# Optimization experiments

Measured on AMD Instinct MI355X. Metric: run time of the kernel, lower is better.

Reference implementation:

```python
import jax, jax.numpy as jnp
import numpy as np
from jax import lax

EPS = 1e-5
K = 32
S1, S2 = 512, 256


def bn_relu(x, gamma, beta, axes):
    # BatchNorm in training mode (batch statistics, biased variance) + ReLU.
    mean = jnp.mean(x, axis=axes, keepdims=True)
    var = jnp.var(x, axis=axes, keepdims=True)
    return jax.nn.relu((x - mean) * lax.rsqrt(var + EPS) * gamma + beta)


def fps(xyz, s):
    # Farthest point sampling, deterministic start at index 0. xyz: [N,3] -> [s] indices
    N = xyz.shape[0]
    def body(carry, _):
        dist, far = carry
        d = jnp.sum((xyz - xyz[far]) ** 2, axis=-1)
        dist = jnp.minimum(dist, d)
        return (dist, jnp.argmax(dist).astype(jnp.int32)), far
    init = (jnp.full((N,), 1e10, xyz.dtype), jnp.int32(0))
    _, idx = lax.scan(body, init, None, length=s)
    return idx


def sample_and_knn_group(s, k, coords, features):
    # coords: [B,N,3], features: [B,N,D]
    fps_idx = jax.vmap(lambda c: fps(c, s))(coords)                      # [B,s]
    new_xyz = jnp.take_along_axis(coords, fps_idx[..., None], axis=1)   # [B,s,3]
    new_feat = jnp.take_along_axis(features, fps_idx[..., None], axis=1)  # [B,s,D]
    # squared euclidean distances [B,s,N]
    d2 = (jnp.sum(new_xyz ** 2, -1)[..., None]
          - 2.0 * jnp.einsum('bsc,bnc->bsn', new_xyz, coords)
          + jnp.sum(coords ** 2, -1)[:, None, :])
    _, knn_idx = lax.top_k(-d2, k)                                       # [B,s,k]
    grouped = jax.vmap(lambda f, i: f[i])(features, knn_idx)             # [B,s,k,D]
    rel = grouped - new_feat[:, :, None, :]
    agg = jnp.concatenate([rel, jnp.broadcast_to(new_feat[:, :, None, :], rel.shape)], axis=-1)  # [B,s,k,2D]
    return new_xyz, agg


def sg_block(s, coords, feats, w1, cb1, g1, b1, w2, cb2, g2, b2):
    new_xyz, agg = sample_and_knn_group(s, K, coords, feats)
    h = bn_relu(jnp.einsum('bskc,oc->bsko', agg, w1) + cb1, g1, b1, (0, 1, 2))
    h = bn_relu(jnp.einsum('bskc,oc->bsko', h, w2) + cb2, g2, b2, (0, 1, 2))
    return new_xyz, jnp.max(h, axis=2)  # max over k neighbors -> [B,s,O]


def setup_inputs() -> dict:
    key = jax.random.key(0)
    ks = jax.random.split(key, 8)
    B, N = 16, 2048
    sc = 0.05
    return {
        'x': jax.random.normal(ks[0], (B, 3, N), jnp.float32),
        'emb_w1': jax.random.normal(ks[1], (64, 3), jnp.float32) * sc,
        'emb_g1': jnp.ones((64,), jnp.float32), 'emb_b1': jnp.zeros((64,), jnp.float32),
        'emb_w2': jax.random.normal(ks[2], (64, 64), jnp.float32) * sc,
        'emb_g2': jnp.ones((64,), jnp.float32), 'emb_b2': jnp.zeros((64,), jnp.float32),
        'sg1_w1': jax.random.normal(ks[3], (128, 128), jnp.float32) * sc,
        'sg1_cb1': jnp.zeros((128,), jnp.float32),
        'sg1_g1': jnp.ones((128,), jnp.float32), 'sg1_b1': jnp.zeros((128,), jnp.float32),
        'sg1_w2': jax.random.normal(ks[4], (128, 128), jnp.float32) * sc,
        'sg1_cb2': jnp.zeros((128,), jnp.float32),
        'sg1_g2': jnp.ones((128,), jnp.float32), 'sg1_b2': jnp.zeros((128,), jnp.float32),
        'sg2_w1': jax.random.normal(ks[5], (512, 256), jnp.float32) * sc,
        'sg2_cb1': jnp.zeros((512,), jnp.float32),
        'sg2_g1': jnp.ones((512,), jnp.float32), 'sg2_b1': jnp.zeros((512,), jnp.float32),
        'sg2_w2': jax.random.normal(ks[6], (512, 512), jnp.float32) * sc,
        'sg2_cb2': jnp.zeros((512,), jnp.float32),
        'sg2_g2': jnp.ones((512,), jnp.float32), 'sg2_b2': jnp.zeros((512,), jnp.float32),
    }


def reference(x, emb_w1, emb_g1, emb_b1, emb_w2, emb_g2, emb_b2,
              sg1_w1, sg1_cb1, sg1_g1, sg1_b1, sg1_w2, sg1_cb2, sg1_g2, sg1_b2,
              sg2_w1, sg2_cb1, sg2_g1, sg2_b1, sg2_w2, sg2_cb2, sg2_g2, sg2_b2):
    xyz = jnp.transpose(x, (0, 2, 1))  # [B,N,3]
    f = bn_relu(jnp.einsum('bnc,oc->bno', xyz, emb_w1), emb_g1, emb_b1, (0, 1))   # [B,N,64]
    f = bn_relu(jnp.einsum('bnc,oc->bno', f, emb_w2), emb_g2, emb_b2, (0, 1))
    xyz1, f1 = sg_block(S1, xyz, f, sg1_w1, sg1_cb1, sg1_g1, sg1_b1,
                        sg1_w2, sg1_cb2, sg1_g2, sg1_b2)   # [B,512,128]
    _, f2 = sg_block(S2, xyz1, f1, sg2_w1, sg2_cb1, sg2_g1, sg2_b1,
                     sg2_w2, sg2_cb2, sg2_g2, sg2_b2)      # [B,256,512]
    return jnp.transpose(f2, (0, 2, 1))  # [B,512,256] to match torch [B,C,s]
```

## Files before the change

### kernel.cpp

```cpp
#include <hip/hip_runtime.h>
#include <hip/hip_bf16.h>

#define EPS_BN 1e-5f
constexpr int BB = 16, NN = 2048, SS1 = 512, SS2 = 256, KNb = 32;

typedef short bf16x8 __attribute__((ext_vector_type(8)));
typedef float f32x4 __attribute__((ext_vector_type(4)));

__device__ inline float bflo(unsigned u) { return __uint_as_float(u << 16); }
__device__ inline float bfhi(unsigned u) { return __uint_as_float(u & 0xffff0000u); }
__device__ inline unsigned short f2bf_bits(float v) {
  __hip_bfloat16 h = __float2bfloat16(v);
  return *reinterpret_cast<unsigned short*>(&h);
}
__device__ inline unsigned fmono(float v) {
  int b = __float_as_int(v);
  return (unsigned)(b ^ ((b >> 31) | 0x80000000));
}

template <int CTRL>
__device__ inline void dpp_step_min(unsigned& hi, unsigned& lo) {
  unsigned hs = (unsigned)__builtin_amdgcn_update_dpp((int)hi, (int)hi, CTRL, 0xF, 0xF, false);
  unsigned ls = (unsigned)__builtin_amdgcn_update_dpp((int)lo, (int)lo, CTRL, 0xF, 0xF, false);
  bool take = (hs < hi) || (hs == hi && ls < lo);
  hi = take ? hs : hi; lo = take ? ls : lo;
}
template <int CTRL>
__device__ inline void dpp_step_maxv_minidx(unsigned& hi, unsigned& lo) {
  unsigned hs = (unsigned)__builtin_amdgcn_update_dpp((int)hi, (int)hi, CTRL, 0xF, 0xF, false);
  unsigned ls = (unsigned)__builtin_amdgcn_update_dpp((int)lo, (int)lo, CTRL, 0xF, 0xF, false);
  bool take = (hs > hi) || (hs == hi && ls < lo);
  hi = take ? hs : hi; lo = take ? ls : lo;
}
__device__ inline void dpp_chain_min(unsigned& hi, unsigned& lo) {
  dpp_step_min<0x111>(hi, lo); dpp_step_min<0x112>(hi, lo);
  dpp_step_min<0x114>(hi, lo); dpp_step_min<0x118>(hi, lo);
  dpp_step_min<0x142>(hi, lo); dpp_step_min<0x143>(hi, lo);
}
__device__ inline void dpp_chain_maxv_minidx(unsigned& hi, unsigned& lo) {
  dpp_step_maxv_minidx<0x111>(hi, lo); dpp_step_maxv_minidx<0x112>(hi, lo);
  dpp_step_maxv_minidx<0x114>(hi, lo); dpp_step_maxv_minidx<0x118>(hi, lo);
  dpp_step_maxv_minidx<0x142>(hi, lo); dpp_step_maxv_minidx<0x143>(hi, lo);
}
__device__ inline int dpp_reduce_min_idx(unsigned hi, unsigned lo) {
  dpp_chain_min(hi, lo);
  return __builtin_amdgcn_readlane((int)lo, 63);
}

__global__ void k_transpose(const float* __restrict__ x, float* __restrict__ xyz) {
  int idx = blockIdx.x * blockDim.x + threadIdx.x;
  if (idx >= BB * NN * 3) return;
  int c = idx % 3; int n = (idx / 3) % NN; int b = idx / (3 * NN);
  xyz[idx] = x[((size_t)b * 3 + c) * NN + n];
}

__global__ void k_emb1(const float* __restrict__ xyz, const float* __restrict__ w,
                       float* __restrict__ out) {
  int idx = blockIdx.x * blockDim.x + threadIdx.x;
  if (idx >= BB * NN * 64) return;
  int o = idx & 63; int pt = idx >> 6;
  const float* p = xyz + (size_t)pt * 3;
  const float* wr = w + o * 3;
  out[idx] = p[0] * wr[0] + p[1] * wr[1] + p[2] * wr[2];
}

__global__ void k_emb2(const float* __restrict__ fin, const float* __restrict__ w,
                       float* __restrict__ out) {
  int idx = blockIdx.x * blockDim.x + threadIdx.x;
  if (idx >= BB * NN * 64) return;
  int o = idx & 63; int pt = idx >> 6;
  const float* f = fin + (size_t)pt * 64;
  const float* wr = w + o * 64;
  float acc = 0.f;
#pragma unroll
  for (int c = 0; c < 64; c++) acc += f[c] * wr[c];
  out[idx] = acc;
}

template <int O>
__global__ void k_stats_direct(const float* __restrict__ data, int rows,
                               const float* __restrict__ gamma, const float* __restrict__ beta,
                               float* __restrict__ scale, float* __restrict__ shift) {
  int o = blockIdx.x; int t = threadIdx.x;
  double s = 0.0, s2 = 0.0;
  for (int r = t; r < rows; r += 256) {
    float v = data[(size_t)r * O + o];
    s += v; s2 += (double)v * (double)v;
  }
  __shared__ double ls[256], ls2[256];
  ls[t] = s; ls2[t] = s2; __syncthreads();
  for (int off = 128; off > 0; off >>= 1) {
    if (t < off) { ls[t] += ls[t + off]; ls2[t] += ls2[t + off]; }
    __syncthreads();
  }
  if (t == 0) {
    double mean = ls[0] / rows;
    double var = ls2[0] / rows - mean * mean;
    float sc = gamma[o] * rsqrtf((float)var + EPS_BN);
    scale[o] = sc; shift[o] = beta[o] - (float)mean * sc;
  }
}

__global__ void k_normrelu(float* __restrict__ data, const float* __restrict__ scale,
                           const float* __restrict__ shift, int total, int O) {
  int idx = blockIdx.x * blockDim.x + threadIdx.x;
  if (idx >= total) return;
  int o = idx % O;
  data[idx] = fmaxf(data[idx] * scale[o] + shift[o], 0.f);
}

template <int N>
__global__ __launch_bounds__(256, 1) void k_fps_mw(const float* __restrict__ xyz, int S,
                                                   int* __restrict__ fpsidx,
                                                   float* __restrict__ newxyz) {
  constexpr int PPL = N / 256;
  int b = blockIdx.x; int t = threadIdx.x;
  int w = t >> 6;
  __shared__ float sx[N], sy[N], sz[N];
  __shared__ unsigned combH[2][4], combL[2][4];
  float px[PPL], py[PPL], pz[PPL], ds[PPL];
#pragma unroll
  for (int r = 0; r < PPL; r++) {
    int i = r * 256 + t;
    size_t base = ((size_t)b * N + i) * 3;
    float xx = xyz[base], yy = xyz[base + 1], zz = xyz[base + 2];
    px[r] = xx; py[r] = yy; pz[r] = zz;
    float ox = xx, oy = yy, oz = zz;
    asm volatile("" : "+v"(ox), "+v"(oy), "+v"(oz));
    sx[i] = ox; sy[i] = oy; sz[i] = oz;
    ds[r] = 1e10f;
  }
  __syncthreads();
  int far = 0; int p = 0;
  for (int it = 0; it < S; it++) {
    float fx = sx[far], fy = sy[far], fz = sz[far];
    if (t == 0) {
      fpsidx[b * S + it] = far;
      size_t ob = ((size_t)b * S + it) * 3;
      newxyz[ob] = fx; newxyz[ob + 1] = fy; newxyz[ob + 2] = fz;
    }
    float mm0 = -1.f, mm1 = -1.f, mm2 = -1.f, mm3 = -1.f;
#pragma unroll
    for (int r = 0; r < PPL; r++) {
      float dx = px[r] - fx, dy = py[r] - fy, dz = pz[r] - fz;
      float d = dx * dx + dy * dy + dz * dz;
      float nd = d < ds[r] ? d : ds[r];
      ds[r] = nd;
      if ((r & 3) == 0) mm0 = nd > mm0 ? nd : mm0;
      else if ((r & 3) == 1) mm1 = nd > mm1 ? nd : mm1;
      else if ((r & 3) == 2) mm2 = nd > mm2 ? nd : mm2;
      else mm3 = nd > mm3 ? nd : mm3;
    }
    float m = fmaxf(fmaxf(mm0, mm1), fmaxf(mm2, mm3));
    int cand[PPL];
#pragma unroll
    for (int r = 0; r < PPL; r++) cand[r] = (ds[r] == m) ? (r * 256 + t) : 0x7fffffff;
#pragma unroll
    for (int st = PPL / 2; st > 0; st >>= 1)
#pragma unroll
      for (int r = 0; r < st; r++) cand[r] = cand[r] < cand[r + st] ? cand[r] : cand[r + st];
    unsigned hi = fmono(m), lo = (unsigned)cand[0];
    dpp_chain_maxv_minidx(hi, lo);
    unsigned rh = (unsigned)__builtin_amdgcn_readlane((int)hi, 63);
    unsigned rl = (unsigned)__builtin_amdgcn_readlane((int)lo, 63);
    combH[p][w] = rh;
    combL[p][w] = rl;
    __syncthreads();
    unsigned bh = combH[p][0], bl = combL[p][0];
#pragma unroll
    for (int ww = 1; ww < 4; ww++) {
      unsigned oh = combH[p][ww], ol = combL[p][ww];
      bool take = (oh > bh) || (oh == bh && ol < bl);
      bh = take ? oh : bh; bl = take ? ol : bl;
    }
    far = (int)bl;
    p ^= 1;
  }
}

template <int N, int S>
__global__ __launch_bounds__(64, 1) void k_knn_wave(const float* __restrict__ pts,
                                                    const float* __restrict__ ctr,
                                                    int* __restrict__ knn) {
  constexpr int PPL = N / 64;
  int blk = blockIdx.x; int lane = threadIdx.x;
  int b = blk / S;
  float cx = ctr[(size_t)blk * 3], cy = ctr[(size_t)blk * 3 + 1], cz = ctr[(size_t)blk * 3 + 2];
  float cn = cx * cx + cy * cy + cz * cz;
  float d2[PPL];
#pragma unroll
  for (int r = 0; r < PPL; r++) {
    int i = r * 64 + lane;
    size_t pb = ((size_t)b * N + i) * 3;
    float xx = pts[pb], yy = pts[pb + 1], zz = pts[pb + 2];
    d2[r] = cn - 2.f * (cx * xx + cy * yy + cz * zz) + (xx * xx + yy * yy + zz * zz);
  }
  for (int kk = 0; kk < KNb; kk++) {
    float a0 = d2[0], a1 = d2[1], a2 = d2[2], a3 = d2[3];
#pragma unroll
    for (int r = 4; r < PPL; r += 4) {
      a0 = fminf(a0, d2[r]); a1 = fminf(a1, d2[r + 1]);
      a2 = fminf(a2, d2[r + 2]); a3 = fminf(a3, d2[r + 3]);
    }
    float m = fminf(fminf(a0, a1), fminf(a2, a3));
    int cand[PPL];
#pragma unroll
    for (int r = 0; r < PPL; r++) cand[r] = (d2[r] == m) ? (r * 64 + lane) : 0x7fffffff;
#pragma unroll
    for (int st = PPL / 2; st > 0; st >>= 1)
#pragma unroll
      for (int r = 0; r < st; r++) cand[r] = cand[r] < cand[r + st] ? cand[r] : cand[r + st];
    int widx = dpp_reduce_min_idx(fmono(m), (unsigned)cand[0]);
    if (lane == 0) knn[(size_t)blk * KNb + kk] = widx;
    int wr = widx >> 6, wl = widx & 63;
#pragma unroll
    for (int r = 0; r < PPL; r++) d2[r] = (r == wr && lane == wl) ? 3.4e38f : d2[r];
  }
}

__global__ void k_f2bf(const float* __restrict__ w, __hip_bfloat16* __restrict__ o, int n) {
  int i = blockIdx.x * blockDim.x + threadIdx.x;
  if (i < n) o[i] = __float2bfloat16(w[i]);
}

template <int D>
__global__ __launch_bounds__(256) void k_gather(const float* __restrict__ feat, int N,
                                                const int* __restrict__ fpsidx,
                                                const int* __restrict__ knn, int S,
                                                __hip_bfloat16* __restrict__ A) {
  int blk = blockIdx.x; int b = blk / S; int t = threadIdx.x;
  __shared__ float cf[D]; __shared__ int nbr[KNb];
  if (t < KNb) nbr[t] = knn[(size_t)blk * KNb + t];
  int center = fpsidx[blk];
  for (int c = t; c < D; c += 256) cf[c] = feat[((size_t)b * N + center) * D + c];
  __syncthreads();
  for (int i = t; i < KNb * D; i += 256) {
    int kk = i / D, c = i - kk * D;
    float v = feat[((size_t)b * N + nbr[kk]) * D + c];
    size_t row = (size_t)blk * KNb + kk;
    A[row * (2 * D) + c] = __float2bfloat16(v - cf[c]);
    A[row * (2 * D) + D + c] = __float2bfloat16(cf[c]);
  }
}

template <int K, int EPI>
__global__ __launch_bounds__(256) void k_mgemm(
    const __hip_bfloat16* __restrict__ A, const __hip_bfloat16* __restrict__ W,
    int N, int Mtiles, const float* __restrict__ bias,
    __hip_bfloat16* __restrict__ Hout,
    float* __restrict__ maxb, float* __restrict__ minb,
    double* __restrict__ rsum, double* __restrict__ rsq) {
  constexpr int SP = 40;
  int bm = blockIdx.x % Mtiles; int bn = blockIdx.x / Mtiles;
  int t = threadIdx.x; int w = t >> 6; int lane = t & 63;
  int wm = w & 1, wn = w >> 1; int quad = lane >> 4; int l15 = lane & 15;
  __shared__ short As[128 * SP];
  __shared__ short Ws[128 * SP];
  f32x4 acc[4][4];
  f32x4 zero = {0.f, 0.f, 0.f, 0.f};
#pragma unroll
  for (int i = 0; i < 4; i++)
#pragma unroll
    for (int j = 0; j < 4; j++) acc[i][j] = zero;

  int srow = t >> 2, sseg = t & 3;
  const short* Ag = (const short*)A;
  const short* Wg = (const short*)W;
  size_t arow0 = (size_t)bm * 128;
  size_t wrow0 = (size_t)bn * 128;

  for (int k0 = 0; k0 < K; k0 += 32) {
    __syncthreads();
    uint4 a0 = *(const uint4*)(Ag + (arow0 + srow) * K + k0 + sseg * 8);
    uint4 a1 = *(const uint4*)(Ag + (arow0 + srow + 64) * K + k0 + sseg * 8);
    uint4 b0 = *(const uint4*)(Wg + (wrow0 + srow) * K + k0 + sseg * 8);
    uint4 b1 = *(const uint4*)(Wg + (wrow0 + srow + 64) * K + k0 + sseg * 8);
    *(uint4*)(As + srow * SP + sseg * 8) = a0;
    *(uint4*)(As + (srow + 64) * SP + sseg * 8) = a1;
    *(uint4*)(Ws + srow * SP + sseg * 8) = b0;
    *(uint4*)(Ws + (srow + 64) * SP + sseg * 8) = b1;
    __syncthreads();
    bf16x8 af[4], bfr[4];
#pragma unroll
    for (int i = 0; i < 4; i++)
      af[i] = *(const bf16x8*)(As + (wm * 64 + i * 16 + l15) * SP + quad * 8);
#pragma unroll
    for (int j = 0; j < 4; j++)
      bfr[j] = *(const bf16x8*)(Ws + (wn * 64 + j * 16 + l15) * SP + quad * 8);
#pragma unroll
    for (int i = 0; i < 4; i++)
#pragma unroll
      for (int j = 0; j < 4; j++)
        acc[i][j] = __builtin_amdgcn_mfma_f32_16x16x32_bf16(af[i], bfr[j], acc[i][j], 0, 0, 0);
  }

  if constexpr (EPI == 0) {
#pragma unroll
    for (int i = 0; i < 4; i++)
#pragma unroll
      for (int j = 0; j < 4; j++) {
        int col = bn * 128 + wn * 64 + j * 16 + l15;
        float bs = bias[col];
#pragma unroll
        for (int r = 0; r < 4; r++) {
          int row = bm * 128 + wm * 64 + i * 16 + quad * 4 + r;
          Hout[(size_t)row * N + col] = __float2bfloat16(acc[i][j][r] + bs);
        }
      }
  } else {
    __shared__ float buf[128][33];
    for (int s = 0; s < 4; s++) {
      __syncthreads();
      if (wn == (s >> 1)) {
        int jb = 2 * (s & 1);
#pragma unroll
        for (int jj = 0; jj < 2; jj++) {
          int j = jb + jj;
          int lcol = jj * 16 + l15;
          float bs = bias[bn * 128 + s * 32 + lcol];
#pragma unroll
          for (int i = 0; i < 4; i++)
#pragma unroll
            for (int r = 0; r < 4; r++)
              buf[wm * 64 + i * 16 + quad * 4 + r][lcol] = acc[i][j][r] + bs;
        }
      }
      __syncthreads();
      if (t < 128) {
        int g = t >> 5, c = t & 31;
        float mx = -3.4e38f, mn = 3.4e38f, su = 0.f, sq = 0.f;
#pragma unroll
        for (int r = 0; r < 32; r++) {
          float v = buf[g * 32 + r][c];
          mx = fmaxf(mx, v); mn = fminf(mn, v);
          su += v; sq += v * v;
        }
        int col = bn * 128 + s * 32 + c;
        size_t gidx = (size_t)bm * 4 + g;
        maxb[gidx * N + col] = mx;
        minb[gidx * N + col] = mn;
        int rep = blockIdx.x & 63;
        atomicAdd(&rsum[(size_t)rep * N + col], (double)su);
        atomicAdd(&rsq[(size_t)rep * N + col], (double)sq);
      }
    }
  }
}

__global__ __launch_bounds__(256) void k_colstats(const __hip_bfloat16* __restrict__ Hm, int O,
                                                  int iters, double* __restrict__ rsum,
                                                  double* __restrict__ rsq) {
  __shared__ float lsum[512], lsq[512];
  int t = threadIdx.x;
  for (int c = t; c < O; c += 256) { lsum[c] = 0.f; lsq[c] = 0.f; }
  __syncthreads();
  size_t base = (size_t)blockIdx.x * 2048 * iters + t * 8;
  float as[8], aq[8];
#pragma unroll
  for (int j = 0; j < 8; j++) { as[j] = 0.f; aq[j] = 0.f; }
  const unsigned* Hu = (const unsigned*)Hm;
  for (int it = 0; it < iters; it++) {
    uint4 raw = *(const uint4*)(Hu + (base + (size_t)it * 2048) / 2);
    unsigned ws_[4] = {raw.x, raw.y, raw.z, raw.w};
#pragma unroll
    for (int k = 0; k < 4; k++) {
      float v0 = bflo(ws_[k]), v1 = bfhi(ws_[k]);
      as[2 * k] += v0; aq[2 * k] += v0 * v0;
      as[2 * k + 1] += v1; aq[2 * k + 1] += v1 * v1;
    }
  }
  int c0 = (t * 8) & (O - 1);
#pragma unroll
  for (int j = 0; j < 8; j++) {
    atomicAdd(&lsum[c0 + j], as[j]);
    atomicAdd(&lsq[c0 + j], aq[j]);
  }
  __syncthreads();
  int rep = blockIdx.x & 63;
  for (int c = t; c < O; c += 256) {
    atomicAdd(&rsum[(size_t)rep * O + c], (double)lsum[c]);
    atomicAdd(&rsq[(size_t)rep * O + c], (double)lsq[c]);
  }
}

__global__ __launch_bounds__(256) void k_bnrelu(__hip_bfloat16* __restrict__ Hm, int O, int iters,
                                                const float* __restrict__ sc,
                                                const float* __restrict__ sh) {
  int t = threadIdx.x;
  size_t base = (size_t)blockIdx.x * 2048 * iters + t * 8;
  int c0 = (t * 8) & (O - 1);
  float s[8], h[8];
#pragma unroll
  for (int j = 0; j < 8; j++) { s[j] = sc[c0 + j]; h[j] = sh[c0 + j]; }
  unsigned* Hu = (unsigned*)Hm;
  for (int it = 0; it < iters; it++) {
    size_t e = (base + (size_t)it * 2048) / 2;
    uint4 raw = *(uint4*)(Hu + e);
    unsigned ws_[4] = {raw.x, raw.y, raw.z, raw.w};
    unsigned out[4];
#pragma unroll
    for (int k = 0; k < 4; k++) {
      float v0 = fmaxf(bflo(ws_[k]) * s[2 * k] + h[2 * k], 0.f);
      float v1 = fmaxf(bfhi(ws_[k]) * s[2 * k + 1] + h[2 * k + 1], 0.f);
      out[k] = (unsigned)f2bf_bits(v0) | ((unsigned)f2bf_bits(v1) << 16);
    }
    uint4 o4 = {out[0], out[1], out[2], out[3]};
    *(uint4*)(Hu + e) = o4;
  }
}

__global__ void k_finalize(const double* __restrict__ rsum, const double* __restrict__ rsq,
                           int O, int rows,
                           const float* __restrict__ gamma, const float* __restrict__ beta,
                           float* __restrict__ scale, float* __restrict__ shift) {
  int o = blockIdx.x * blockDim.x + threadIdx.x;
  if (o >= O) return;
  double s = 0, s2 = 0;
  for (int r = 0; r < 64; r++) { s += rsum[(size_t)r * O + o]; s2 += rsq[(size_t)r * O + o]; }
  double mean = s / rows;
  double var = s2 / rows - mean * mean;
  float sc = gamma[o] * rsqrtf((float)var + EPS_BN);
  scale[o] = sc; shift[o] = beta[o] - (float)mean * sc;
}

__global__ void k_final_feat(const float* __restrict__ maxb, const float* __restrict__ minb,
                             const float* __restrict__ scale, const float* __restrict__ shift,
                             float* __restrict__ out, int total, int O) {
  int idx = blockIdx.x * blockDim.x + threadIdx.x;
  if (idx >= total) return;
  int o = idx % O; float sc = scale[o];
  float sel = sc > 0.f ? maxb[idx] : minb[idx];
  out[idx] = fmaxf(sel * sc + shift[o], 0.f);
}

__global__ void k_final_out(const float* __restrict__ maxb, const float* __restrict__ minb,
                            const float* __restrict__ scale, const float* __restrict__ shift,
                            float* __restrict__ out) {
  int idx = blockIdx.x * blockDim.x + threadIdx.x;
  if (idx >= BB * SS2 * 512) return;
  int o = idx % 512; int si = (idx / 512) % SS2; int b = idx / (512 * SS2);
  float sc = scale[o];
  float sel = sc > 0.f ? maxb[idx] : minb[idx];
  out[((size_t)b * 512 + o) * SS2 + si] = fmaxf(sel * sc + shift[o], 0.f);
}

extern "C" void kernel_launch(void* const* d_in, const int* in_sizes, int n_in,
                              void* d_out, int out_size, void* d_ws, size_t ws_size,
                              hipStream_t stream) {
  const float* x       = (const float*)d_in[0];
  const float* emb_w1  = (const float*)d_in[1];
  const float* emb_g1  = (const float*)d_in[2];
  const float* emb_b1  = (const float*)d_in[3];
  const float* emb_w2  = (const float*)d_in[4];
  const float* emb_g2  = (const float*)d_in[5];
  const float* emb_b2  = (const float*)d_in[6];
  const float* sg1_w1  = (const float*)d_in[7];
  const float* sg1_cb1 = (const float*)d_in[8];
  const float* sg1_g1  = (const float*)d_in[9];
  const float* sg1_b1  = (const float*)d_in[10];
  const float* sg1_w2  = (const float*)d_in[11];
  const float* sg1_cb2 = (const float*)d_in[12];
  const float* sg1_g2  = (const float*)d_in[13];
  const float* sg1_b2  = (const float*)d_in[14];
  const float* sg2_w1  = (const float*)d_in[15];
  const float* sg2_cb1 = (const float*)d_in[16];
  const float* sg2_g1  = (const float*)d_in[17];
  const float* sg2_b1  = (const float*)d_in[18];
  const float* sg2_w2  = (const float*)d_in[19];
  const float* sg2_cb2 = (const float*)d_in[20];
  const float* sg2_g2  = (const float*)d_in[21];
  const float* sg2_b2  = (const float*)d_in[22];

  char* ws = (char*)d_ws;
  size_t off = 0;
  auto alloc = [&](size_t bytes) -> size_t {
    size_t cur = off; off += (bytes + 255) & ~(size_t)255; return cur;
  };
  float* xyz  = (float*)(ws + alloc((size_t)BB * NN * 3 * 4));
  float* fA   = (float*)(ws + alloc((size_t)BB * NN * 64 * 4));
  float* fB   = (float*)(ws + alloc((size_t)BB * NN * 64 * 4));
  float* f1   = (float*)(ws + alloc((size_t)BB * SS1 * 128 * 4));
  float* nx1  = (float*)(ws + alloc((size_t)BB * SS1 * 3 * 4));
  float* nx2  = (float*)(ws + alloc((size_t)BB * SS2 * 3 * 4));
  int* fps1   = (int*)(ws + alloc((size_t)BB * SS1 * 4));
  int* fps2   = (int*)(ws + alloc((size_t)BB * SS2 * 4));
  int* knn1   = (int*)(ws + alloc((size_t)BB * SS1 * KNb * 4));
  int* knn2   = (int*)(ws + alloc((size_t)BB * SS2 * KNb * 4));
  float* maxb = (float*)(ws + alloc((size_t)BB * SS2 * 512 * 4));
  float* minb = (float*)(ws + alloc((size_t)BB * SS2 * 512 * 4));
  float* scbuf = (float*)(ws + alloc((size_t)12 * 512 * 4));
  float* sc11 = scbuf + 4 * 512, *sh11 = scbuf + 5 * 512;
  float* sc12 = scbuf + 6 * 512, *sh12 = scbuf + 7 * 512;
  float* sc21 = scbuf + 8 * 512, *sh21 = scbuf + 9 * 512;
  float* sc22 = scbuf + 10 * 512, *sh22 = scbuf + 11 * 512;
  float* sc_e1 = scbuf + 0 * 512, *sh_e1 = scbuf + 1 * 512;
  float* sc_e2 = scbuf + 2 * 512, *sh_e2 = scbuf + 3 * 512;
  size_t statsz = (size_t)8 * 64 * 512 * 8;
  char* statz = ws + alloc(statsz);
  double* st = (double*)statz;
  double* rsA = st + 0 * 64 * 512, *rqA = st + 1 * 64 * 512;
  double* rsB = st + 2 * 64 * 512, *rqB = st + 3 * 64 * 512;
  double* rsC = st + 4 * 64 * 512, *rqC = st + 5 * 64 * 512;
  double* rsD = st + 6 * 64 * 512, *rqD = st + 7 * 64 * 512;
  __hip_bfloat16* wb11 = (__hip_bfloat16*)(ws + alloc(128 * 128 * 2));
  __hip_bfloat16* wb12 = (__hip_bfloat16*)(ws + alloc(128 * 128 * 2));
  __hip_bfloat16* wb21 = (__hip_bfloat16*)(ws + alloc(512 * 256 * 2));
  __hip_bfloat16* wb22 = (__hip_bfloat16*)(ws + alloc(512 * 512 * 2));
  __hip_bfloat16* Abuf = (__hip_bfloat16*)(ws + alloc((size_t)262144 * 128 * 2));
  __hip_bfloat16* Hbuf = (__hip_bfloat16*)(ws + alloc((size_t)131072 * 512 * 2));

  hipMemsetAsync(statz, 0, statsz, stream);

  const int thr = 256;
  k_transpose<<<(BB * NN * 3 + thr - 1) / thr, thr, 0, stream>>>(x, xyz);
  k_emb1<<<(BB * NN * 64 + thr - 1) / thr, thr, 0, stream>>>(xyz, emb_w1, fA);
  k_stats_direct<64><<<64, 256, 0, stream>>>(fA, BB * NN, emb_g1, emb_b1, sc_e1, sh_e1);
  k_normrelu<<<(BB * NN * 64 + thr - 1) / thr, thr, 0, stream>>>(fA, sc_e1, sh_e1, BB * NN * 64, 64);
  k_emb2<<<(BB * NN * 64 + thr - 1) / thr, thr, 0, stream>>>(fA, emb_w2, fB);
  k_stats_direct<64><<<64, 256, 0, stream>>>(fB, BB * NN, emb_g2, emb_b2, sc_e2, sh_e2);
  k_normrelu<<<(BB * NN * 64 + thr - 1) / thr, thr, 0, stream>>>(fB, sc_e2, sh_e2, BB * NN * 64, 64);

  k_f2bf<<<(128 * 128 + 255) / 256, 256, 0, stream>>>(sg1_w1, wb11, 128 * 128);
  k_f2bf<<<(128 * 128 + 255) / 256, 256, 0, stream>>>(sg1_w2, wb12, 128 * 128);
  k_f2bf<<<(512 * 256 + 255) / 256, 256, 0, stream>>>(sg2_w1, wb21, 512 * 256);
  k_f2bf<<<(512 * 512 + 255) / 256, 256, 0, stream>>>(sg2_w2, wb22, 512 * 512);

  k_fps_mw<NN><<<BB, 256, 0, stream>>>(xyz, SS1, fps1, nx1);
  k_knn_wave<NN, SS1><<<BB * SS1, 64, 0, stream>>>(xyz, nx1, knn1);

  k_gather<64><<<BB * SS1, 256, 0, stream>>>(fB, NN, fps1, knn1, SS1, Abuf);
  k_mgemm<128, 0><<<2048, 256, 0, stream>>>(Abuf, wb11, 128, 2048, sg1_cb1, Hbuf,
                                            nullptr, nullptr, nullptr, nullptr);
  k_colstats<<<1024, 256, 0, stream>>>(Hbuf, 128, 16, rsA, rqA);
  k_finalize<<<1, 128, 0, stream>>>(rsA, rqA, 128, 262144, sg1_g1, sg1_b1, sc11, sh11);
  k_bnrelu<<<1024, 256, 0, stream>>>(Hbuf, 128, 16, sc11, sh11);
  k_mgemm<128, 1><<<2048, 256, 0, stream>>>(Hbuf, wb12, 128, 2048, sg1_cb2, nullptr,
                                            maxb, minb, rsB, rqB);
  k_finalize<<<1, 128, 0, stream>>>(rsB, rqB, 128, 262144, sg1_g2, sg1_b2, sc12, sh12);
  k_final_feat<<<(BB * SS1 * 128 + thr - 1) / thr, thr, 0, stream>>>(maxb, minb, sc12, sh12,
                                                                     f1, BB * SS1 * 128, 128);

  k_fps_mw<SS1><<<BB, 256, 0, stream>>>(nx1, SS2, fps2, nx2);
  k_knn_wave<SS1, SS2><<<BB * SS2, 64, 0, stream>>>(nx1, nx2, knn2);

  k_gather<128><<<BB * SS2, 256, 0, stream>>>(f1, SS1, fps2, knn2, SS2, Abuf);
  k_mgemm<256, 0><<<1024 * 4, 256, 0, stream>>>(Abuf, wb21, 512, 1024, sg2_cb1, Hbuf,
                                                nullptr, nullptr, nullptr, nullptr);
  k_colstats<<<2048, 256, 0, stream>>>(Hbuf, 512, 16, rsC, rqC);
  k_finalize<<<4, 128, 0, stream>>>(rsC, rqC, 512, 131072, sg2_g1, sg2_b1, sc21, sh21);
  k_bnrelu<<<2048, 256, 0, stream>>>(Hbuf, 512, 16, sc21, sh21);
  k_mgemm<512, 1><<<1024 * 4, 256, 0, stream>>>(Hbuf, wb22, 512, 1024, sg2_cb2, nullptr,
                                                maxb, minb, rsD, rqD);
  k_finalize<<<4, 128, 0, stream>>>(rsD, rqD, 512, 131072, sg2_g2, sg2_b2, sc22, sh22);
  k_final_out<<<(BB * SS2 * 512 + thr - 1) / thr, thr, 0, stream>>>(maxb, minb, sc22, sh22,
                                                                    (float*)d_out);
}
```

Baseline: 1.429 ms.

## Fuse BN column stats into GEMM epilogue, parallelize embedding stats, streamline FPS argmax

The first-layer GEMMs of both SG blocks now accumulate per-column sum and sum-of-squares in their epilogue and push them with double atomics, which removes the separate column-stats pass that re-read the bf16 activation buffer. The embedding BatchNorm stats switch from 64 blocks doing strided column reads to 256 blocks doing coalesced float4 reads with shared-memory and global atomic partials, followed by the existing finalize kernel. FPS tracks the argmax index alongside the running max, so the second candidate scan per iteration goes away. Costs are more atomic traffic in the GEMM epilogue and stats computed from fp32 values before bf16 rounding, which differs slightly from the old stats taken on rounded data.

```diff
diff --git a/kernel.cpp b/kernel.cpp
--- a/kernel.cpp
+++ b/kernel.cpp
@@ -77,27 +77,32 @@
   out[idx] = acc;
 }
 
-template <int O>
-__global__ void k_stats_direct(const float* __restrict__ data, int rows,
-                               const float* __restrict__ gamma, const float* __restrict__ beta,
-                               float* __restrict__ scale, float* __restrict__ shift) {
-  int o = blockIdx.x; int t = threadIdx.x;
-  double s = 0.0, s2 = 0.0;
-  for (int r = t; r < rows; r += 256) {
-    float v = data[(size_t)r * O + o];
-    s += v; s2 += (double)v * (double)v;
-  }
-  __shared__ double ls[256], ls2[256];
-  ls[t] = s; ls2[t] = s2; __syncthreads();
-  for (int off = 128; off > 0; off >>= 1) {
-    if (t < off) { ls[t] += ls[t + off]; ls2[t] += ls2[t + off]; }
-    __syncthreads();
-  }
-  if (t == 0) {
-    double mean = ls[0] / rows;
-    double var = ls2[0] / rows - mean * mean;
-    float sc = gamma[o] * rsqrtf((float)var + EPS_BN);
-    scale[o] = sc; shift[o] = beta[o] - (float)mean * sc;
+__global__ __launch_bounds__(256) void k_stats_co(const float* __restrict__ d,
+                                                  double* __restrict__ rsum,
+                                                  double* __restrict__ rsq) {
+  __shared__ float ls[64], lq[64];
+  int t = threadIdx.x;
+  if (t < 64) { ls[t] = 0.f; lq[t] = 0.f; }
+  __syncthreads();
+  size_t base = (size_t)blockIdx.x * 8192 + t * 4;
+  float a0 = 0, a1 = 0, a2 = 0, a3 = 0, q0 = 0, q1 = 0, q2 = 0, q3 = 0;
+  for (int it = 0; it < 8; it++) {
+    float4 v = *(const float4*)(d + base + (size_t)it * 1024);
+    a0 += v.x; q0 += v.x * v.x;
+    a1 += v.y; q1 += v.y * v.y;
+    a2 += v.z; q2 += v.z * v.z;
+    a3 += v.w; q3 += v.w * v.w;
+  }
+  int c0 = (t * 4) & 63;
+  atomicAdd(&ls[c0], a0); atomicAdd(&lq[c0], q0);
+  atomicAdd(&ls[c0 + 1], a1); atomicAdd(&lq[c0 + 1], q1);
+  atomicAdd(&ls[c0 + 2], a2); atomicAdd(&lq[c0 + 2], q2);
+  atomicAdd(&ls[c0 + 3], a3); atomicAdd(&lq[c0 + 3], q3);
+  __syncthreads();
+  if (t < 64) {
+    int rep = blockIdx.x & 63;
+    atomicAdd(&rsum[(size_t)rep * 64 + t], (double)ls[t]);
+    atomicAdd(&rsq[(size_t)rep * 64 + t], (double)lq[t]);
   }
 }
 
@@ -139,27 +144,28 @@
       size_t ob = ((size_t)b * S + it) * 3;
       newxyz[ob] = fx; newxyz[ob + 1] = fy; newxyz[ob + 2] = fz;
     }
-    float mm0 = -1.f, mm1 = -1.f, mm2 = -1.f, mm3 = -1.f;
+    float mv0 = -1.f, mv1 = -1.f, mv2 = -1.f, mv3 = -1.f;
+    int mi0 = 0, mi1 = 0, mi2 = 0, mi3 = 0;
 #pragma unroll
     for (int r = 0; r < PPL; r++) {
       float dx = px[r] - fx, dy = py[r] - fy, dz = pz[r] - fz;
       float d = dx * dx + dy * dy + dz * dz;
       float nd = d < ds[r] ? d : ds[r];
       ds[r] = nd;
-      if ((r & 3) == 0) mm0 = nd > mm0 ? nd : mm0;
-      else if ((r & 3) == 1) mm1 = nd > mm1 ? nd : mm1;
-      else if ((r & 3) == 2) mm2 = nd > mm2 ? nd : mm2;
-      else mm3 = nd > mm3 ? nd : mm3;
-    }
-    float m = fmaxf(fmaxf(mm0, mm1), fmaxf(mm2, mm3));
-    int cand[PPL];
-#pragma unroll
-    for (int r = 0; r < PPL; r++) cand[r] = (ds[r] == m) ? (r * 256 + t) : 0x7fffffff;
-#pragma unroll
-    for (int st = PPL / 2; st > 0; st >>= 1)
-#pragma unroll
-      for (int r = 0; r < st; r++) cand[r] = cand[r] < cand[r + st] ? cand[r] : cand[r + st];
-    unsigned hi = fmono(m), lo = (unsigned)cand[0];
+      int gi = r * 256 + t;
+      if ((r & 3) == 0) { bool tk = nd > mv0; mv0 = tk ? nd : mv0; mi0 = tk ? gi : mi0; }
+      else if ((r & 3) == 1) { bool tk = nd > mv1; mv1 = tk ? nd : mv1; mi1 = tk ? gi : mi1; }
+      else if ((r & 3) == 2) { bool tk = nd > mv2; mv2 = tk ? nd : mv2; mi2 = tk ? gi : mi2; }
+      else { bool tk = nd > mv3; mv3 = tk ? nd : mv3; mi3 = tk ? gi : mi3; }
+    }
+    { bool tk = (mv1 > mv0) || (mv1 == mv0 && mi1 < mi0);
+      mv0 = tk ? mv1 : mv0; mi0 = tk ? mi1 : mi0; }
+    { bool tk = (mv3 > mv2) || (mv3 == mv2 && mi3 < mi2);
+      mv2 = tk ? mv3 : mv2; mi2 = tk ? mi3 : mi2; }
+    { bool tk = (mv2 > mv0) || (mv2 == mv0 && mi2 < mi0);
+      mv0 = tk ? mv2 : mv0; mi0 = tk ? mi2 : mi0; }
+    unsigned hi = __float_as_uint(mv0);
+    unsigned lo = (unsigned)mi0;
     dpp_chain_maxv_minidx(hi, lo);
     unsigned rh = (unsigned)__builtin_amdgcn_readlane((int)hi, 63);
     unsigned rl = (unsigned)__builtin_amdgcn_readlane((int)lo, 63);
@@ -295,18 +301,24 @@
   }
 
   if constexpr (EPI == 0) {
-#pragma unroll
-    for (int i = 0; i < 4; i++)
-#pragma unroll
-      for (int j = 0; j < 4; j++) {
-        int col = bn * 128 + wn * 64 + j * 16 + l15;
-        float bs = bias[col];
+    int rep = blockIdx.x & 63;
+#pragma unroll
+    for (int j = 0; j < 4; j++) {
+      int col = bn * 128 + wn * 64 + j * 16 + l15;
+      float bs = bias[col];
+      float su = 0.f, sq = 0.f;
+#pragma unroll
+      for (int i = 0; i < 4; i++)
 #pragma unroll
         for (int r = 0; r < 4; r++) {
           int row = bm * 128 + wm * 64 + i * 16 + quad * 4 + r;
-          Hout[(size_t)row * N + col] = __float2bfloat16(acc[i][j][r] + bs);
+          float v = acc[i][j][r] + bs;
+          Hout[(size_t)row * N + col] = __float2bfloat16(v);
+          su += v; sq += v * v;
         }
-      }
+      atomicAdd(&rsum[(size_t)rep * N + col], (double)su);
+      atomicAdd(&rsq[(size_t)rep * N + col], (double)sq);
+    }
   } else {
     __shared__ float buf[128][33];
     for (int s = 0; s < 4; s++) {
@@ -344,42 +356,6 @@
         atomicAdd(&rsq[(size_t)rep * N + col], (double)sq);
       }
     }
-  }
-}
-
-__global__ __launch_bounds__(256) void k_colstats(const __hip_bfloat16* __restrict__ Hm, int O,
-                                                  int iters, double* __restrict__ rsum,
-                                                  double* __restrict__ rsq) {
-  __shared__ float lsum[512], lsq[512];
-  int t = threadIdx.x;
-  for (int c = t; c < O; c += 256) { lsum[c] = 0.f; lsq[c] = 0.f; }
-  __syncthreads();
-  size_t base = (size_t)blockIdx.x * 2048 * iters + t * 8;
-  float as[8], aq[8];
-#pragma unroll
-  for (int j = 0; j < 8; j++) { as[j] = 0.f; aq[j] = 0.f; }
-  const unsigned* Hu = (const unsigned*)Hm;
-  for (int it = 0; it < iters; it++) {
-    uint4 raw = *(const uint4*)(Hu + (base + (size_t)it * 2048) / 2);
-    unsigned ws_[4] = {raw.x, raw.y, raw.z, raw.w};
-#pragma unroll
-    for (int k = 0; k < 4; k++) {
-      float v0 = bflo(ws_[k]), v1 = bfhi(ws_[k]);
-      as[2 * k] += v0; aq[2 * k] += v0 * v0;
-      as[2 * k + 1] += v1; aq[2 * k + 1] += v1 * v1;
-    }
-  }
-  int c0 = (t * 8) & (O - 1);
-#pragma unroll
-  for (int j = 0; j < 8; j++) {
-    atomicAdd(&lsum[c0 + j], as[j]);
-    atomicAdd(&lsq[c0 + j], aq[j]);
-  }
-  __syncthreads();
-  int rep = blockIdx.x & 63;
-  for (int c = t; c < O; c += 256) {
-    atomicAdd(&rsum[(size_t)rep * O + c], (double)lsum[c]);
-    atomicAdd(&rsq[(size_t)rep * O + c], (double)lsq[c]);
   }
 }
 
@@ -495,13 +471,15 @@
   float* sc22 = scbuf + 10 * 512, *sh22 = scbuf + 11 * 512;
   float* sc_e1 = scbuf + 0 * 512, *sh_e1 = scbuf + 1 * 512;
   float* sc_e2 = scbuf + 2 * 512, *sh_e2 = scbuf + 3 * 512;
-  size_t statsz = (size_t)8 * 64 * 512 * 8;
+  size_t statsz = (size_t)12 * 64 * 512 * 8;
   char* statz = ws + alloc(statsz);
   double* st = (double*)statz;
   double* rsA = st + 0 * 64 * 512, *rqA = st + 1 * 64 * 512;
   double* rsB = st + 2 * 64 * 512, *rqB = st + 3 * 64 * 512;
   double* rsC = st + 4 * 64 * 512, *rqC = st + 5 * 64 * 512;
   double* rsD = st + 6 * 64 * 512, *rqD = st + 7 * 64 * 512;
+  double* rsE1 = st + 8 * 64 * 512, *rqE1 = st + 9 * 64 * 512;
+  double* rsE2 = st + 10 * 64 * 512, *rqE2 = st + 11 * 64 * 512;
   __hip_bfloat16* wb11 = (__hip_bfloat16*)(ws + alloc(128 * 128 * 2));
   __hip_bfloat16* wb12 = (__hip_bfloat16*)(ws + alloc(128 * 128 * 2));
   __hip_bfloat16* wb21 = (__hip_bfloat16*)(ws + alloc(512 * 256 * 2));
@@ -514,10 +492,12 @@
   const int thr = 256;
   k_transpose<<<(BB * NN * 3 + thr - 1) / thr, thr, 0, stream>>>(x, xyz);
   k_emb1<<<(BB * NN * 64 + thr - 1) / thr, thr, 0, stream>>>(xyz, emb_w1, fA);
-  k_stats_direct<64><<<64, 256, 0, stream>>>(fA, BB * NN, emb_g1, emb_b1, sc_e1, sh_e1);
+  k_stats_co<<<256, 256, 0, stream>>>(fA, rsE1, rqE1);
+  k_finalize<<<1, 64, 0, stream>>>(rsE1, rqE1, 64, BB * NN, emb_g1, emb_b1, sc_e1, sh_e1);
   k_normrelu<<<(BB * NN * 64 + thr - 1) / thr, thr, 0, stream>>>(fA, sc_e1, sh_e1, BB * NN * 64, 64);
   k_emb2<<<(BB * NN * 64 + thr - 1) / thr, thr, 0, stream>>>(fA, emb_w2, fB);
-  k_stats_direct<64><<<64, 256, 0, stream>>>(fB, BB * NN, emb_g2, emb_b2, sc_e2, sh_e2);
+  k_stats_co<<<256, 256, 0, stream>>>(fB, rsE2, rqE2);
+  k_finalize<<<1, 64, 0, stream>>>(rsE2, rqE2, 64, BB * NN, emb_g2, emb_b2, sc_e2, sh_e2);
   k_normrelu<<<(BB * NN * 64 + thr - 1) / thr, thr, 0, stream>>>(fB, sc_e2, sh_e2, BB * NN * 64, 64);
 
   k_f2bf<<<(128 * 128 + 255) / 256, 256, 0, stream>>>(sg1_w1, wb11, 128 * 128);
@@ -530,8 +510,7 @@
 
   k_gather<64><<<BB * SS1, 256, 0, stream>>>(fB, NN, fps1, knn1, SS1, Abuf);
   k_mgemm<128, 0><<<2048, 256, 0, stream>>>(Abuf, wb11, 128, 2048, sg1_cb1, Hbuf,
-                                            nullptr, nullptr, nullptr, nullptr);
-  k_colstats<<<1024, 256, 0, stream>>>(Hbuf, 128, 16, rsA, rqA);
+                                            nullptr, nullptr, rsA, rqA);
   k_finalize<<<1, 128, 0, stream>>>(rsA, rqA, 128, 262144, sg1_g1, sg1_b1, sc11, sh11);
   k_bnrelu<<<1024, 256, 0, stream>>>(Hbuf, 128, 16, sc11, sh11);
   k_mgemm<128, 1><<<2048, 256, 0, stream>>>(Hbuf, wb12, 128, 2048, sg1_cb2, nullptr,
@@ -545,8 +524,7 @@
 
   k_gather<128><<<BB * SS2, 256, 0, stream>>>(f1, SS1, fps2, knn2, SS2, Abuf);
   k_mgemm<256, 0><<<1024 * 4, 256, 0, stream>>>(Abuf, wb21, 512, 1024, sg2_cb1, Hbuf,
-                                                nullptr, nullptr, nullptr, nullptr);
-  k_colstats<<<2048, 256, 0, stream>>>(Hbuf, 512, 16, rsC, rqC);
+                                                nullptr, nullptr, rsC, rqC);
   k_finalize<<<4, 128, 0, stream>>>(rsC, rqC, 512, 131072, sg2_g1, sg2_b1, sc21, sh21);
   k_bnrelu<<<2048, 256, 0, stream>>>(Hbuf, 512, 16, sc21, sh21);
   k_mgemm<512, 1><<<1024 * 4, 256, 0, stream>>>(Hbuf, wb22, 512, 1024, sg2_cb2, nullptr,
```

After: 1.465 ms. 2.5% more time.
